# Performance work log

Measured on AMD Instinct MI355X. Metric: run time of the kernel, lower is better.

The kernel has to match this reference:

```python
import jax, jax.numpy as jnp
import numpy as np

TOP_K = 8
N_GROUP = 8
TOPK_GROUP = 4
ROUTED_SCALING_FACTOR = 2.5
NORM_TOPK_PROB = True
TOKENS = 16384
HIDDEN = 4096
N_EXPERTS = 256


def setup_inputs() -> dict:
    key = jax.random.key(0)
    k1, k2, k3 = jax.random.split(key, 3)
    x = jax.random.normal(k1, (TOKENS, HIDDEN), dtype=jnp.float32)
    weight = jax.random.normal(k2, (N_EXPERTS, HIDDEN), dtype=jnp.float32) * 0.02
    e_score_correction_bias = jax.random.normal(k3, (N_EXPERTS,), dtype=jnp.float32) * 0.01
    return {"x": x, "weight": weight, "e_score_correction_bias": e_score_correction_bias}


def reference(x, weight, e_score_correction_bias):
    # gates: [T, E]
    gates = x @ weight.T
    orig_scores = jax.nn.sigmoid(gates.astype(jnp.float32))
    scores = orig_scores + e_score_correction_bias
    T, E = scores.shape
    eg = E // N_GROUP  # experts per group
    s = scores.reshape(T, N_GROUP, eg)
    # group score = sum of top-2 expert scores within each group -> [T, G]
    group_scores = jax.lax.top_k(s, 2)[0].sum(axis=-1)
    # torch code selects the (n_group - topk_group) SMALLEST groups and keeps
    # only those (masked_fill zeroes everything else) -- replicate faithfully.
    k_drop = N_GROUP - TOPK_GROUP
    _, bottom_idx = jax.lax.top_k(-group_scores, k_drop)  # [T, k_drop]
    keep = jnp.zeros((T, N_GROUP), dtype=bool).at[jnp.arange(T)[:, None], bottom_idx].set(True)
    s = jnp.where(keep[:, :, None], s, 0.0).reshape(T, E)
    # torch.topk(-scores) -> indices of the k SMALLEST scores
    _, inds = jax.lax.top_k(-s, TOP_K)  # [T, top_k]
    sel = jnp.take_along_axis(orig_scores, inds, axis=-1)
    if TOP_K > 1 and NORM_TOPK_PROB:
        sel = sel / (sel.sum(axis=-1, keepdims=True) + 1e-20)
    sel = sel * ROUTED_SCALING_FACTOR
    return inds, sel
```

## Files before the change

### kernel.cpp

```cpp
#include <hip/hip_runtime.h>
#include <hip/hip_fp16.h>
#include <cstdint>
#include <cmath>

#define TOKENS  16384
#define HIDDEN  4096
#define NEXP    256
#define TOPK    8
#define KDROP   4

typedef _Float16 f16x8  __attribute__((ext_vector_type(8)));
typedef float    f32x16 __attribute__((ext_vector_type(16)));

#define LO_SCALE 2048.0f
#define LO_INV   (1.0f/2048.0f)

#define WS_GATES_OFF 0
#define WS_WH_OFF    16777216
#define WS_WL_OFF    18874368

__global__ __launch_bounds__(256)
void wsplit(const float* __restrict__ w, _Float16* __restrict__ wh,
            _Float16* __restrict__ wl)
{
    const int idx = blockIdx.x * 256 + threadIdx.x;
    const int e   = idx >> 9;
    const int kg8 = idx & 511;
    const float4* p = (const float4*)(w + (size_t)e * HIDDEN + kg8 * 8);
    float4 f0 = p[0], f1 = p[1];
    float v[8] = {f0.x, f0.y, f0.z, f0.w, f1.x, f1.y, f1.z, f1.w};
    f16x8 hi, lo;
    #pragma unroll
    for (int i = 0; i < 8; ++i) {
        _Float16 h = (_Float16)v[i];
        hi[i] = h;
        lo[i] = (_Float16)((v[i] - (float)h) * LO_SCALE);
    }
    const int kc = kg8 >> 2, s = (kg8 >> 1) & 1, hl = kg8 & 1;
    const int cid = ((kc * 2 + s) * 8 + (e >> 5)) * 64 + hl * 32 + (e & 31);
    ((f16x8*)wh)[cid] = hi;
    ((f16x8*)wl)[cid] = lo;
}

__global__ __launch_bounds__(256, 2)
void gemm_split(const float* __restrict__ x, const _Float16* __restrict__ wh,
                const _Float16* __restrict__ wl, float* __restrict__ gates)
{
    __shared__ _Float16 Ah[64 * 32];
    __shared__ _Float16 Al[64 * 32];

    const int tid  = threadIdx.x;
    const int wv   = tid >> 6;
    const int lane = tid & 63;
    const int tok0 = blockIdx.x * 64;
    const int kcg0 = blockIdx.y * 64;

    const int sm = tid >> 2;
    const int sq = tid & 3;
    const float* xr = x + (size_t)(tok0 + sm) * HIDDEN;
    const int scid = ((sq >> 1) * 2 + (sm >> 5)) * 64 + (sq & 1) * 32 + (sm & 31);

    const f16x8* whc = (const f16x8*)wh;
    const f16x8* wlc = (const f16x8*)wl;

    f32x16 accH[2][2] = {};
    f32x16 accX[2][2] = {};

    for (int kc = 0; kc < 64; ++kc) {
        const int kcg = kcg0 + kc;
        const float4* ap = (const float4*)(xr + kcg * 32 + sq * 8);
        float4 f0 = ap[0];
        float4 f1 = ap[1];
        f16x8 bh[2][2], bl[2][2];
        #pragma unroll
        for (int s = 0; s < 2; ++s) {
            const int base = ((kcg * 2 + s) * 8 + wv * 2) * 64 + lane;
            bh[s][0] = whc[base];
            bh[s][1] = whc[base + 64];
            bl[s][0] = wlc[base];
            bl[s][1] = wlc[base + 64];
        }

        __syncthreads();

        {
            float v[8] = {f0.x, f0.y, f0.z, f0.w, f1.x, f1.y, f1.z, f1.w};
            f16x8 hi, lo;
            #pragma unroll
            for (int i = 0; i < 8; ++i) {
                _Float16 h = (_Float16)v[i];
                hi[i] = h;
                lo[i] = (_Float16)((v[i] - (float)h) * LO_SCALE);
            }
            *(f16x8*)&Ah[scid * 8] = hi;
            *(f16x8*)&Al[scid * 8] = lo;
        }

        __syncthreads();

        #pragma unroll
        for (int s = 0; s < 2; ++s) {
            f16x8 ah0 = *(const f16x8*)&Ah[((s * 2 + 0) * 64 + lane) * 8];
            f16x8 ah1 = *(const f16x8*)&Ah[((s * 2 + 1) * 64 + lane) * 8];
            f16x8 al0 = *(const f16x8*)&Al[((s * 2 + 0) * 64 + lane) * 8];
            f16x8 al1 = *(const f16x8*)&Al[((s * 2 + 1) * 64 + lane) * 8];

            accH[0][0] = __builtin_amdgcn_mfma_f32_32x32x16_f16(ah0, bh[s][0], accH[0][0], 0, 0, 0);
            accH[0][1] = __builtin_amdgcn_mfma_f32_32x32x16_f16(ah0, bh[s][1], accH[0][1], 0, 0, 0);
            accH[1][0] = __builtin_amdgcn_mfma_f32_32x32x16_f16(ah1, bh[s][0], accH[1][0], 0, 0, 0);
            accH[1][1] = __builtin_amdgcn_mfma_f32_32x32x16_f16(ah1, bh[s][1], accH[1][1], 0, 0, 0);
            accX[0][0] = __builtin_amdgcn_mfma_f32_32x32x16_f16(al0, bh[s][0], accX[0][0], 0, 0, 0);
            accX[0][1] = __builtin_amdgcn_mfma_f32_32x32x16_f16(al0, bh[s][1], accX[0][1], 0, 0, 0);
            accX[1][0] = __builtin_amdgcn_mfma_f32_32x32x16_f16(al1, bh[s][0], accX[1][0], 0, 0, 0);
            accX[1][1] = __builtin_amdgcn_mfma_f32_32x32x16_f16(al1, bh[s][1], accX[1][1], 0, 0, 0);
            accX[0][0] = __builtin_amdgcn_mfma_f32_32x32x16_f16(ah0, bl[s][0], accX[0][0], 0, 0, 0);
            accX[0][1] = __builtin_amdgcn_mfma_f32_32x32x16_f16(ah0, bl[s][1], accX[0][1], 0, 0, 0);
            accX[1][0] = __builtin_amdgcn_mfma_f32_32x32x16_f16(ah1, bl[s][0], accX[1][0], 0, 0, 0);
            accX[1][1] = __builtin_amdgcn_mfma_f32_32x32x16_f16(ah1, bl[s][1], accX[1][1], 0, 0, 0);
        }
    }

    const int col   = lane & 31;
    const int rbase = 4 * (lane >> 5);
    #pragma unroll
    for (int r = 0; r < 2; ++r)
        #pragma unroll
        for (int c = 0; c < 2; ++c) {
            float* gp = gates + (size_t)(tok0 + r * 32) * NEXP + wv * 64 + c * 32 + col;
            #pragma unroll
            for (int reg = 0; reg < 16; ++reg) {
                const int row = (reg & 3) + 8 * (reg >> 2) + rbase;
                atomicAdd(gp + (size_t)row * NEXP,
                          accH[r][c][reg] + accX[r][c][reg] * LO_INV);
            }
        }
}

__device__ __forceinline__ unsigned ordkey(float f) {
    unsigned u = __float_as_uint(f);
    return (u & 0x80000000u) ? ~u : (u | 0x80000000u);
}

__global__ __launch_bounds__(256, 4)
void gate_epilogue(const float* __restrict__ gates,
                   const float* __restrict__ bias,
                   float* __restrict__ out)
{
    const int tid  = threadIdx.x;
    const int wv   = tid >> 6;
    const int lane = tid & 63;
    const int t    = blockIdx.x * 4 + wv;

    float4 gv = ((const float4*)(gates + (size_t)t * NEXP))[lane];
    float4 bv = ((const float4*)bias)[lane];

    float sig0 = 1.0f / (1.0f + expf(-gv.x));
    float sig1 = 1.0f / (1.0f + expf(-gv.y));
    float sig2 = 1.0f / (1.0f + expf(-gv.z));
    float sig3 = 1.0f / (1.0f + expf(-gv.w));
    float sc0 = sig0 + bv.x, sc1 = sig1 + bv.y;
    float sc2 = sig2 + bv.z, sc3 = sig3 + bv.w;

    float m1 = fmaxf(sc0, sc1);
    float m2 = fminf(sc0, sc1);
    if (sc2 > m1) { m2 = m1; m1 = sc2; } else m2 = fmaxf(m2, sc2);
    if (sc3 > m1) { m2 = m1; m1 = sc3; } else m2 = fmaxf(m2, sc3);
    #pragma unroll
    for (int off = 1; off < 8; off <<= 1) {
        float o1 = __shfl_xor(m1, off);
        float o2 = __shfl_xor(m2, off);
        float nm1 = fmaxf(m1, o1);
        float nm2 = fmaxf(fminf(m1, o1), fmaxf(m2, o2));
        m1 = nm1; m2 = nm2;
    }
    float gsum = m1 + m2;
    float gs[8];
    #pragma unroll
    for (int gi = 0; gi < 8; ++gi) gs[gi] = __shfl(gsum, gi * 8);

    int keepmask = 0;
    #pragma unroll
    for (int g = 0; g < 8; ++g) {
        int rank = 0;
        #pragma unroll
        for (int h = 0; h < 8; ++h)
            rank += (gs[h] < gs[g]) || (gs[h] == gs[g] && h < g);
        if (rank < KDROP) keepmask |= (1 << g);
    }
    const bool kept = (keepmask >> (lane >> 3)) & 1;

    const unsigned ib = (unsigned)(lane * 4);
    unsigned long long k0 = ((unsigned long long)ordkey(kept ? sc0 : 0.0f) << 32) | (ib + 0);
    unsigned long long k1 = ((unsigned long long)ordkey(kept ? sc1 : 0.0f) << 32) | (ib + 1);
    unsigned long long k2 = ((unsigned long long)ordkey(kept ? sc2 : 0.0f) << 32) | (ib + 2);
    unsigned long long k3 = ((unsigned long long)ordkey(kept ? sc3 : 0.0f) << 32) | (ib + 3);

    float ssum = 0.0f, myval = 0.0f;
    int myidx = 0;
    #pragma unroll
    for (int r = 0; r < TOPK; ++r) {
        unsigned long long kmin = k0 < k1 ? k0 : k1;
        if (k2 < kmin) kmin = k2;
        if (k3 < kmin) kmin = k3;
        #pragma unroll
        for (int off = 32; off >= 1; off >>= 1) {
            unsigned long long o = __shfl_xor(kmin, off);
            if (o < kmin) kmin = o;
        }
        const int id   = (int)(kmin & 0xffffffffull);
        const int src  = id >> 2;
        const int slot = id & 3;
        float vsrc = (slot == 0) ? sig0 : (slot == 1) ? sig1
                   : (slot == 2) ? sig2 : sig3;
        float v = __shfl(vsrc, src);
        ssum += v;
        if (lane == r) { myidx = id; myval = v; }
        const bool mine = (lane == src);
        if (mine && slot == 0) k0 = ~0ull;
        if (mine && slot == 1) k1 = ~0ull;
        if (mine && slot == 2) k2 = ~0ull;
        if (mine && slot == 3) k3 = ~0ull;
    }

    if (lane < TOPK) {
        out[(size_t)t * TOPK + lane] = (float)myidx;
        out[(size_t)TOKENS * TOPK + (size_t)t * TOPK + lane] =
            myval / (ssum + 1e-20f) * 2.5f;
    }
}

extern "C" void kernel_launch(void* const* d_in, const int* in_sizes, int n_in,
                              void* d_out, int out_size, void* d_ws, size_t ws_size,
                              hipStream_t stream)
{
    const float* x    = (const float*)d_in[0];
    const float* w    = (const float*)d_in[1];
    const float* bias = (const float*)d_in[2];
    float* out = (float*)d_out;

    float*     gates = (float*)((char*)d_ws + WS_GATES_OFF);
    _Float16*  wh    = (_Float16*)((char*)d_ws + WS_WH_OFF);
    _Float16*  wl    = (_Float16*)((char*)d_ws + WS_WL_OFF);

    hipMemsetAsync(gates, 0, (size_t)TOKENS * NEXP * sizeof(float), stream);
    wsplit<<<dim3(512), dim3(256), 0, stream>>>(w, wh, wl);
    gemm_split<<<dim3(TOKENS / 64, 2), dim3(256), 0, stream>>>(x, wh, wl, gates);
    gate_epilogue<<<dim3(TOKENS / 4), dim3(256), 0, stream>>>(gates, bias, out);
}
```

Baseline: 446.9 us.

## Double-buffer GEMM LDS tiles and replace atomic split-K with two partial buffers

The GEMM main loop now double-buffers the A tiles in shared memory and prefetches the next chunk's x and weight fragments into registers while the current MFMAs run, which halves the barriers per iteration. The two K-halves write plain stores into separate partial-gate buffers instead of atomically adding into one zeroed buffer. That removes the memset and the atomics, and the epilogue sums the two partials. The cost is more register pressure from the prefetched fragments, double the LDS, and an extra 16 MB buffer read in the epilogue.

New measurement: 431.3 us. -3.5%, faster.

```diff
diff --git a/kernel.cpp b/kernel.cpp
--- a/kernel.cpp
+++ b/kernel.cpp
@@ -15,9 +15,10 @@
 #define LO_SCALE 2048.0f
 #define LO_INV   (1.0f/2048.0f)
 
-#define WS_GATES_OFF 0
-#define WS_WH_OFF    16777216
-#define WS_WL_OFF    18874368
+#define WS_G0_OFF 0
+#define WS_G1_OFF 16777216
+#define WS_WH_OFF 33554432
+#define WS_WL_OFF 35651584
 
 __global__ __launch_bounds__(256)
 void wsplit(const float* __restrict__ w, _Float16* __restrict__ wh,
@@ -44,16 +45,18 @@
 
 __global__ __launch_bounds__(256, 2)
 void gemm_split(const float* __restrict__ x, const _Float16* __restrict__ wh,
-                const _Float16* __restrict__ wl, float* __restrict__ gates)
-{
-    __shared__ _Float16 Ah[64 * 32];
-    __shared__ _Float16 Al[64 * 32];
+                const _Float16* __restrict__ wl,
+                float* __restrict__ g0, float* __restrict__ g1)
+{
+    __shared__ _Float16 Ah[2][64 * 32];
+    __shared__ _Float16 Al[2][64 * 32];
 
     const int tid  = threadIdx.x;
     const int wv   = tid >> 6;
     const int lane = tid & 63;
     const int tok0 = blockIdx.x * 64;
     const int kcg0 = blockIdx.y * 64;
+    float* gates_half = blockIdx.y ? g1 : g0;
 
     const int sm = tid >> 2;
     const int sq = tid & 3;
@@ -66,44 +69,61 @@
     f32x16 accH[2][2] = {};
     f32x16 accX[2][2] = {};
 
-    for (int kc = 0; kc < 64; ++kc) {
-        const int kcg = kcg0 + kc;
-        const float4* ap = (const float4*)(xr + kcg * 32 + sq * 8);
+    f16x8 bh[2][2], bl[2][2];
+
+    {
+        const float4* ap = (const float4*)(xr + kcg0 * 32 + sq * 8);
         float4 f0 = ap[0];
         float4 f1 = ap[1];
-        f16x8 bh[2][2], bl[2][2];
         #pragma unroll
         for (int s = 0; s < 2; ++s) {
-            const int base = ((kcg * 2 + s) * 8 + wv * 2) * 64 + lane;
+            const int base = ((kcg0 * 2 + s) * 8 + wv * 2) * 64 + lane;
             bh[s][0] = whc[base];
             bh[s][1] = whc[base + 64];
             bl[s][0] = wlc[base];
             bl[s][1] = wlc[base + 64];
         }
-
-        __syncthreads();
-
-        {
-            float v[8] = {f0.x, f0.y, f0.z, f0.w, f1.x, f1.y, f1.z, f1.w};
-            f16x8 hi, lo;
-            #pragma unroll
-            for (int i = 0; i < 8; ++i) {
-                _Float16 h = (_Float16)v[i];
-                hi[i] = h;
-                lo[i] = (_Float16)((v[i] - (float)h) * LO_SCALE);
-            }
-            *(f16x8*)&Ah[scid * 8] = hi;
-            *(f16x8*)&Al[scid * 8] = lo;
-        }
-
-        __syncthreads();
+        float v[8] = {f0.x, f0.y, f0.z, f0.w, f1.x, f1.y, f1.z, f1.w};
+        f16x8 hi, lo;
+        #pragma unroll
+        for (int i = 0; i < 8; ++i) {
+            _Float16 h = (_Float16)v[i];
+            hi[i] = h;
+            lo[i] = (_Float16)((v[i] - (float)h) * LO_SCALE);
+        }
+        *(f16x8*)&Ah[0][scid * 8] = hi;
+        *(f16x8*)&Al[0][scid * 8] = lo;
+    }
+    __syncthreads();
+
+    #pragma unroll 2
+    for (int kc = 0; kc < 64; ++kc) {
+        const int cur  = kc & 1;
+        const bool more = (kc < 63);
+
+        float4 a0n, a1n;
+        f16x8 bhn[2][2], bln[2][2];
+        if (more) {
+            const int kcg = kcg0 + kc + 1;
+            const float4* ap = (const float4*)(xr + kcg * 32 + sq * 8);
+            a0n = ap[0];
+            a1n = ap[1];
+            #pragma unroll
+            for (int s = 0; s < 2; ++s) {
+                const int base = ((kcg * 2 + s) * 8 + wv * 2) * 64 + lane;
+                bhn[s][0] = whc[base];
+                bhn[s][1] = whc[base + 64];
+                bln[s][0] = wlc[base];
+                bln[s][1] = wlc[base + 64];
+            }
+        }
 
         #pragma unroll
         for (int s = 0; s < 2; ++s) {
-            f16x8 ah0 = *(const f16x8*)&Ah[((s * 2 + 0) * 64 + lane) * 8];
-            f16x8 ah1 = *(const f16x8*)&Ah[((s * 2 + 1) * 64 + lane) * 8];
-            f16x8 al0 = *(const f16x8*)&Al[((s * 2 + 0) * 64 + lane) * 8];
-            f16x8 al1 = *(const f16x8*)&Al[((s * 2 + 1) * 64 + lane) * 8];
+            f16x8 ah0 = *(const f16x8*)&Ah[cur][((s * 2 + 0) * 64 + lane) * 8];
+            f16x8 ah1 = *(const f16x8*)&Ah[cur][((s * 2 + 1) * 64 + lane) * 8];
+            f16x8 al0 = *(const f16x8*)&Al[cur][((s * 2 + 0) * 64 + lane) * 8];
+            f16x8 al1 = *(const f16x8*)&Al[cur][((s * 2 + 1) * 64 + lane) * 8];
 
             accH[0][0] = __builtin_amdgcn_mfma_f32_32x32x16_f16(ah0, bh[s][0], accH[0][0], 0, 0, 0);
             accH[0][1] = __builtin_amdgcn_mfma_f32_32x32x16_f16(ah0, bh[s][1], accH[0][1], 0, 0, 0);
@@ -118,6 +138,25 @@
             accX[1][0] = __builtin_amdgcn_mfma_f32_32x32x16_f16(ah1, bl[s][0], accX[1][0], 0, 0, 0);
             accX[1][1] = __builtin_amdgcn_mfma_f32_32x32x16_f16(ah1, bl[s][1], accX[1][1], 0, 0, 0);
         }
+
+        if (more) {
+            float v[8] = {a0n.x, a0n.y, a0n.z, a0n.w, a1n.x, a1n.y, a1n.z, a1n.w};
+            f16x8 hi, lo;
+            #pragma unroll
+            for (int i = 0; i < 8; ++i) {
+                _Float16 h = (_Float16)v[i];
+                hi[i] = h;
+                lo[i] = (_Float16)((v[i] - (float)h) * LO_SCALE);
+            }
+            *(f16x8*)&Ah[cur ^ 1][scid * 8] = hi;
+            *(f16x8*)&Al[cur ^ 1][scid * 8] = lo;
+            #pragma unroll
+            for (int s = 0; s < 2; ++s) {
+                bh[s][0] = bhn[s][0]; bh[s][1] = bhn[s][1];
+                bl[s][0] = bln[s][0]; bl[s][1] = bln[s][1];
+            }
+        }
+        __syncthreads();
     }
 
     const int col   = lane & 31;
@@ -126,12 +165,11 @@
     for (int r = 0; r < 2; ++r)
         #pragma unroll
         for (int c = 0; c < 2; ++c) {
-            float* gp = gates + (size_t)(tok0 + r * 32) * NEXP + wv * 64 + c * 32 + col;
+            float* gp = gates_half + (size_t)(tok0 + r * 32) * NEXP + wv * 64 + c * 32 + col;
             #pragma unroll
             for (int reg = 0; reg < 16; ++reg) {
                 const int row = (reg & 3) + 8 * (reg >> 2) + rbase;
-                atomicAdd(gp + (size_t)row * NEXP,
-                          accH[r][c][reg] + accX[r][c][reg] * LO_INV);
+                gp[(size_t)row * NEXP] = accH[r][c][reg] + accX[r][c][reg] * LO_INV;
             }
         }
 }
@@ -142,7 +180,8 @@
 }
 
 __global__ __launch_bounds__(256, 4)
-void gate_epilogue(const float* __restrict__ gates,
+void gate_epilogue(const float* __restrict__ g0,
+                   const float* __restrict__ g1,
                    const float* __restrict__ bias,
                    float* __restrict__ out)
 {
@@ -151,8 +190,10 @@
     const int lane = tid & 63;
     const int t    = blockIdx.x * 4 + wv;
 
-    float4 gv = ((const float4*)(gates + (size_t)t * NEXP))[lane];
+    float4 ga = ((const float4*)(g0 + (size_t)t * NEXP))[lane];
+    float4 gb = ((const float4*)(g1 + (size_t)t * NEXP))[lane];
     float4 bv = ((const float4*)bias)[lane];
+    float4 gv = make_float4(ga.x + gb.x, ga.y + gb.y, ga.z + gb.z, ga.w + gb.w);
 
     float sig0 = 1.0f / (1.0f + expf(-gv.x));
     float sig1 = 1.0f / (1.0f + expf(-gv.y));
@@ -238,12 +279,12 @@
     const float* bias = (const float*)d_in[2];
     float* out = (float*)d_out;
 
-    float*     gates = (float*)((char*)d_ws + WS_GATES_OFF);
-    _Float16*  wh    = (_Float16*)((char*)d_ws + WS_WH_OFF);
-    _Float16*  wl    = (_Float16*)((char*)d_ws + WS_WL_OFF);
-
-    hipMemsetAsync(gates, 0, (size_t)TOKENS * NEXP * sizeof(float), stream);
+    float*     g0 = (float*)((char*)d_ws + WS_G0_OFF);
+    float*     g1 = (float*)((char*)d_ws + WS_G1_OFF);
+    _Float16*  wh = (_Float16*)((char*)d_ws + WS_WH_OFF);
+    _Float16*  wl = (_Float16*)((char*)d_ws + WS_WL_OFF);
+
     wsplit<<<dim3(512), dim3(256), 0, stream>>>(w, wh, wl);
-    gemm_split<<<dim3(TOKENS / 64, 2), dim3(256), 0, stream>>>(x, wh, wl, gates);
-    gate_epilogue<<<dim3(TOKENS / 4), dim3(256), 0, stream>>>(gates, bias, out);
-}
+    gemm_split<<<dim3(TOKENS / 64, 2), dim3(256), 0, stream>>>(x, wh, wl, g0, g1);
+    gate_epilogue<<<dim3(TOKENS / 4), dim3(256), 0, stream>>>(g0, g1, bias, out);
+}
```
